# Kernel optimization log

Measured on AMD Instinct MI355X. Metric: run time of the kernel, lower is better.

## Reference

```python
import jax, jax.numpy as jnp
import numpy as np

D_MODEL = 1024
NUM_HEADS = 16
THETA = 10000.0


def _trunc_normal(key, shape):
    # matches torch.nn.init.trunc_normal_(std=std, a=-3*std, b=3*std)
    std = (2.0 / (shape[0] + shape[1])) ** 0.5
    return jax.random.truncated_normal(key, -3.0, 3.0, shape, dtype=jnp.float32) * std


def setup_inputs() -> dict:
    key = jax.random.key(0)
    kx, kq, kk, kv, ko = jax.random.split(key, 5)
    B, S, D = 2, 2048, D_MODEL
    return {
        "x": jax.random.normal(kx, (B, S, D), dtype=jnp.float32),
        "Wq": _trunc_normal(kq, (D, D)),  # torch Linear weight: [out, in]
        "Wk": _trunc_normal(kk, (D, D)),
        "Wv": _trunc_normal(kv, (D, D)),
        "Wo": _trunc_normal(ko, (D, D)),
        "token_positions": jnp.arange(S, dtype=jnp.int32),
    }


def _rope(x, token_positions):
    # x: [B, H, S, d_k]; RoPE on interleaved pairs (k r) with r=2
    d_k = x.shape[-1]
    inv_freq = THETA ** (-2.0 * jnp.arange(d_k // 2, dtype=jnp.float32) / d_k)
    ang = token_positions.astype(jnp.float32)[:, None] * inv_freq[None, :]  # [S, d_k/2]
    sin, cos = jnp.sin(ang).astype(x.dtype), jnp.cos(ang).astype(x.dtype)
    x0, x1 = x[..., 0::2], x[..., 1::2]
    y0 = x0 * cos - x1 * sin
    y1 = x0 * sin + x1 * cos
    return jnp.stack([y0, y1], axis=-1).reshape(x.shape)


def reference(x, Wq, Wk, Wv, Wo, token_positions):
    B, S, D = x.shape
    H = NUM_HEADS
    d_k = D // H

    def proj(W):  # y = x @ W^T, split heads -> [B, H, S, d_k]
        y = jnp.einsum('bsd,ed->bse', x, W)
        return y.reshape(B, S, H, d_k).transpose(0, 2, 1, 3)

    q = _rope(proj(Wq), token_positions)
    k = _rope(proj(Wk), token_positions)
    v = proj(Wv)

    # causal mask: attend where pos_k <= pos_q
    mask = token_positions[None, :] <= token_positions[:, None]  # [S_q, S_k]
    logits = jnp.einsum('bhqd,bhkd->bhqk', q, k) / (d_k ** 0.5)
    logits = jnp.where(mask, logits, -jnp.inf)
    scores = jax.nn.softmax(logits, axis=-1)
    attn = jnp.einsum('bhqk,bhkd->bhqd', scores, v)  # [B, H, S, d_k]
    attn = attn.transpose(0, 2, 1, 3).reshape(B, S, D)
    return jnp.einsum('bsd,ed->bse', attn, Wo)
```

## Files before the change

### kernel.cpp

```cpp
#include <hip/hip_runtime.h>
#include <hip/hip_bf16.h>

typedef __attribute__((ext_vector_type(8))) short s16x8;
typedef __attribute__((ext_vector_type(4))) float f32x4;

__device__ __forceinline__ unsigned short f2b(float x) {
  unsigned int u = __float_as_uint(x);
  u = (u + 0x7fffu + ((u >> 16) & 1u)) >> 16;
  return (unsigned short)u;
}

__device__ __forceinline__ float b2f(unsigned short u) {
  return __uint_as_float((unsigned int)u << 16);
}

__device__ __forceinline__ unsigned int cvtpk(float a, float b) {
  unsigned int r;
  asm("v_cvt_pk_bf16_f32 %0, %1, %2" : "=v"(r) : "v"(a), "v"(b));
  return r;
}

#if __has_builtin(__builtin_amdgcn_exp2f)
__device__ __forceinline__ float fexp2(float x) { return __builtin_amdgcn_exp2f(x); }
#else
__device__ __forceinline__ float fexp2(float x) { return exp2f(x); }
#endif

__device__ __forceinline__ void gl2lds16(const unsigned short* g, unsigned short* lds) {
  __builtin_amdgcn_global_load_lds(
      (const __attribute__((address_space(1))) unsigned int*)g,
      (__attribute__((address_space(3))) unsigned int*)lds, 16, 0, 0);
}

#define QSCALE 0.18033688011f

__global__ __launch_bounds__(256) void cast_all(
    const float* __restrict__ x,  const float* __restrict__ Wq,
    const float* __restrict__ Wk, const float* __restrict__ Wv,
    const float* __restrict__ Wo, unsigned short* __restrict__ dst) {
  int i = blockIdx.x * 256 + threadIdx.x;
  const float* src;
  int off;
  if (i < 1048576) { src = x; off = i; }
  else {
    int j = i - 1048576;
    int seg = j >> 18;
    off = j & 262143;
    src = (seg == 0) ? Wq : (seg == 1) ? Wk : (seg == 2) ? Wv : Wo;
  }
  const float4 v = ((const float4*)src)[off];
  uint2 o;
  o.x = cvtpk(v.x, v.y);
  o.y = cvtpk(v.z, v.w);
  ((uint2*)dst)[i] = o;
}

#define KDIM 1024

__global__ __launch_bounds__(256, 4) void gemm_qkv(
    const unsigned short* __restrict__ A,
    const unsigned short* __restrict__ Bt,
    const int* __restrict__ tok,
    unsigned short* __restrict__ Qo,
    unsigned short* __restrict__ Ko,
    unsigned short* __restrict__ Vt) {
  __shared__ unsigned short As[2][128 * 32];
  __shared__ unsigned short Bs[2][128 * 32];
  const int tid = threadIdx.x;
  const int bid = blockIdx.x;
  const int xcd = bid & 7;
  const int loc = bid >> 3;
  const int m0 = (loc / 3) * 128;
  const int n0 = (xcd * 3 + loc % 3) * 128;
  const int w = tid >> 6, lane = tid & 63;
  const int ln = lane & 15, quad = lane >> 4;
  const int wm = (w >> 1) * 64, wn = (w & 1) * 64;

  const int rr = lane >> 2;
  const int gsw = ((lane & 3) ^ ((rr ^ (rr >> 2)) & 3)) * 8;
  const int sr = (ln ^ (ln >> 2)) & 3;

  const f32x4 zero = {0.f, 0.f, 0.f, 0.f};
  f32x4 acc[4][4];
#pragma unroll
  for (int i = 0; i < 4; ++i)
#pragma unroll
    for (int j = 0; j < 4; ++j) acc[i][j] = zero;

#define QKV_STAGE(kb, p)                                                              \
  do {                                                                                \
    int col = (kb) * 32 + gsw;                                                        \
    gl2lds16(A  + (size_t)(m0 + w * 32 + rr) * KDIM + col,      &As[p][(w * 32) * 32]);      \
    gl2lds16(A  + (size_t)(m0 + w * 32 + 16 + rr) * KDIM + col, &As[p][(w * 32 + 16) * 32]); \
    gl2lds16(Bt + (size_t)(n0 + w * 32 + rr) * KDIM + col,      &Bs[p][(w * 32) * 32]);      \
    gl2lds16(Bt + (size_t)(n0 + w * 32 + 16 + rr) * KDIM + col, &Bs[p][(w * 32 + 16) * 32]); \
  } while (0)

  QKV_STAGE(0, 0);
  for (int kb = 0; kb < 32; ++kb) {
    const int p = kb & 1;
    __syncthreads();
    if (kb < 31) QKV_STAGE(kb + 1, p ^ 1);
    s16x8 af[4], bfr[4];
#pragma unroll
    for (int i = 0; i < 4; ++i)
      af[i] = *(const s16x8*)(&As[p][(wm + i * 16 + ln) * 32 + ((quad ^ sr) * 8)]);
#pragma unroll
    for (int j = 0; j < 4; ++j)
      bfr[j] = *(const s16x8*)(&Bs[p][(wn + j * 16 + ln) * 32 + ((quad ^ sr) * 8)]);
#pragma unroll
    for (int i = 0; i < 4; ++i)
#pragma unroll
      for (int j = 0; j < 4; ++j)
        acc[i][j] = __builtin_amdgcn_mfma_f32_16x16x32_bf16(af[i], bfr[j], acc[i][j], 0, 0, 0);
  }
#undef QKV_STAGE

  __syncthreads();
  const bool isV = (n0 >= 2048);
  if (!isV) {
    const float qs = (n0 + wn < 1024) ? QSCALE : 1.0f;
    const int gnb = n0 + wn;
    const int h = (gnb & 1023) >> 6;
    unsigned short* dst = (gnb < 1024) ? Qo : Ko;
    unsigned short* T = &As[0][0] + w * 1088;
    float invj[4];
#pragma unroll
    for (int j = 0; j < 4; ++j)
      invj[j] = __expf(-0.2878231366f * (float)((j * 16 + ln) >> 1));
#pragma unroll
    for (int i = 0; i < 4; ++i) {
      const int mb = m0 + wm + i * 16;
      const int b = mb >> 11;
      const int sb = mb & 2047;
#pragma unroll
      for (int j = 0; j < 4; ++j) {
        const int dd = j * 16 + ln;
#pragma unroll
        for (int r = 0; r < 4; ++r) {
          float val = acc[i][j][r];
          float part = __shfl_xor(val, 1, 64);
          int s = sb + quad * 4 + r;
          float ang = (float)s * invj[j];
          float sn, cs;
          __sincosf(ang, &sn, &cs);
          float x0 = (dd & 1) ? part : val;
          float x1 = (dd & 1) ? val : part;
          float y = (dd & 1) ? (x0 * sn + x1 * cs) : (x0 * cs - x1 * sn);
          T[(quad * 4 + r) * 68 + dd] = f2b(y * qs);
        }
      }
      __builtin_amdgcn_wave_barrier();
      const size_t obase = ((size_t)(b * 16 + h) * 2048 + sb) * 64;
#pragma unroll
      for (int ss = 0; ss < 16; ++ss)
        dst[obase + (size_t)ss * 64 + lane] = T[ss * 68 + lane];
      __builtin_amdgcn_wave_barrier();
    }
  } else {
    unsigned short* T = &As[0][0] + w * 1120;
    const int b = m0 >> 11;
    const int hrow = ((n0 - 2048) + wn) >> 6;
    const int s0 = (m0 & 2047) + wm;
    const size_t vbase = (size_t)(b * 16 + hrow) * 64;
#pragma unroll
    for (int j = 0; j < 4; ++j) {
#pragma unroll
      for (int i = 0; i < 4; ++i)
#pragma unroll
        for (int r = 0; r < 4; ++r)
          T[ln * 70 + i * 16 + quad * 4 + r] = f2b(acc[i][j][r]);
      __builtin_amdgcn_wave_barrier();
#pragma unroll
      for (int dd = 0; dd < 16; ++dd)
        Vt[(vbase + j * 16 + dd) * 2048 + s0 + lane] = T[dd * 70 + lane];
      __builtin_amdgcn_wave_barrier();
    }
  }
}

__global__ __launch_bounds__(256, 3) void attn_partial(
    const unsigned short* __restrict__ Q,
    const unsigned short* __restrict__ K,
    const unsigned short* __restrict__ Vt,
    unsigned short* __restrict__ Opart,
    float2* __restrict__ ML) {
  __shared__ unsigned short Ks[2][64 * 64];
  __shared__ unsigned short Vs[2][64 * 64];
  __shared__ unsigned short Pt[4][16 * 64];

  const int bid = blockIdx.x;
  const int xcd = bid & 7;
  const int loc = bid >> 3;
  const int bh = xcd * 4 + (loc & 3);
  const int widx = loc >> 2;
  int c, qh;
  if (widx < 28) {
    if (widx < 13)      { c = 0; qh = 3 + widx; }
    else if (widx < 22) { c = 1; qh = 7 + (widx - 13); }
    else if (widx < 27) { c = 2; qh = 11 + (widx - 22); }
    else                { c = 3; qh = 15; }
  } else {
    int s = widx - 28;
    int wt = s >> 2;
    c = s & 3;
    qh = 4 * c + 2 - wt;
  }
  const int kbeg = c * 512;
  const int khi = min(kbeg + 512, qh * 128 + 128);
  const int nit = (khi - kbeg) >> 6;

  const int tid = threadIdx.x;
  const int w = tid >> 6, lane = tid & 63;
  const int ln = lane & 15, quad = lane >> 4;
  const int qb = qh * 128 + w * 32;

  const unsigned short* Qb = Q + (size_t)bh * 2048 * 64;
  const unsigned short* Kb = K + (size_t)bh * 2048 * 64;
  const unsigned short* Vb = Vt + (size_t)bh * 64 * 2048;

  const int srow = w * 16 + (lane >> 3);
  const int sg = (lane & 7) ^ (srow & 7);

#define ATTN_STAGE(k0, p)                                                            \
  do {                                                                               \
    gl2lds16(Kb + (size_t)((k0) + srow) * 64 + sg * 8,       &Ks[p][(w * 16) * 64]);      \
    gl2lds16(Kb + (size_t)((k0) + srow + 8) * 64 + sg * 8,   &Ks[p][(w * 16 + 8) * 64]);  \
    gl2lds16(Vb + (size_t)srow * 2048 + (k0) + sg * 8,       &Vs[p][(w * 16) * 64]);      \
    gl2lds16(Vb + (size_t)(srow + 8) * 2048 + (k0) + sg * 8, &Vs[p][(w * 16 + 8) * 64]);  \
  } while (0)

  s16x8 bq[2][2];
#pragma unroll
  for (int u = 0; u < 2; ++u)
#pragma unroll
    for (int hh = 0; hh < 2; ++hh)
      bq[u][hh] = *(const s16x8*)(&Qb[(size_t)(qb + u * 16 + ln) * 64 + hh * 32 + quad * 8]);

  const f32x4 zero = {0.f, 0.f, 0.f, 0.f};
  f32x4 o[2][4];
#pragma unroll
  for (int u = 0; u < 2; ++u)
#pragma unroll
    for (int j = 0; j < 4; ++j) o[u][j] = zero;
  float m_i[2] = {-3e38f, -3e38f};
  float l_i[2] = {0.f, 0.f};

  const int rdsw = ((ln & 7) * 8);
  unsigned char* ptb = (unsigned char*)&Pt[w][0];
  const int pswz = (ln & 7) << 4;

  ATTN_STAGE(kbeg, 0);
  for (int it = 0; it < nit; ++it) {
    const int p = it & 1;
    const int k0 = kbeg + it * 64;
    __syncthreads();
    if (it + 1 < nit) ATTN_STAGE(k0 + 64, p ^ 1);

    if (k0 <= qb + 31) {
      s16x8 ka[4][2];
#pragma unroll
      for (int t = 0; t < 4; ++t)
#pragma unroll
        for (int hh = 0; hh < 2; ++hh)
          ka[t][hh] = *(const s16x8*)(&Ks[p][(t * 16 + ln) * 64 + (((hh * 4 + quad) * 8) ^ rdsw)]);

#pragma unroll
      for (int u = 0; u < 2; ++u) {
        const int qlo = qb + u * 16;
        if (k0 > qlo + 15) continue;
        f32x4 st[4];
#pragma unroll
        for (int t = 0; t < 4; ++t) {
          f32x4 s = __builtin_amdgcn_mfma_f32_16x16x32_bf16(ka[t][0], bq[u][0], zero, 0, 0, 0);
          st[t] = __builtin_amdgcn_mfma_f32_16x16x32_bf16(ka[t][1], bq[u][1], s, 0, 0, 0);
        }
        float lm = -3e38f;
        if (k0 + 63 > qlo) {
          const int q = qlo + ln;
#pragma unroll
          for (int t = 0; t < 4; ++t)
#pragma unroll
            for (int r = 0; r < 4; ++r) {
              int kk = k0 + t * 16 + quad * 4 + r;
              float v = st[t][r];
              v = (kk > q) ? -3e38f : v;
              st[t][r] = v;
              lm = fmaxf(lm, v);
            }
        } else {
#pragma unroll
          for (int t = 0; t < 4; ++t)
#pragma unroll
            for (int r = 0; r < 4; ++r) lm = fmaxf(lm, st[t][r]);
        }
        lm = fmaxf(lm, __shfl_xor(lm, 16, 64));
        lm = fmaxf(lm, __shfl_xor(lm, 32, 64));

        float rs = 0.f;
        if (__all(lm <= m_i[u])) {
          const float mn = m_i[u];
#pragma unroll
          for (int t = 0; t < 4; ++t)
#pragma unroll
            for (int r = 0; r < 4; ++r) {
              float pv = fexp2(st[t][r] - mn);
              st[t][r] = pv;
              rs += pv;
            }
          rs += __shfl_xor(rs, 16, 64);
          rs += __shfl_xor(rs, 32, 64);
          l_i[u] += rs;
        } else {
          const float mn = fmaxf(m_i[u], lm);
          const float al = fexp2(m_i[u] - mn);
#pragma unroll
          for (int t = 0; t < 4; ++t)
#pragma unroll
            for (int r = 0; r < 4; ++r) {
              float pv = fexp2(st[t][r] - mn);
              st[t][r] = pv;
              rs += pv;
            }
          rs += __shfl_xor(rs, 16, 64);
          rs += __shfl_xor(rs, 32, 64);
          m_i[u] = mn;
          l_i[u] = l_i[u] * al + rs;
#pragma unroll
          for (int j = 0; j < 4; ++j) o[u][j] *= al;
        }

#pragma unroll
        for (int t = 0; t < 4; ++t) {
          uint2 pv;
          pv.x = cvtpk(st[t][0], st[t][1]);
          pv.y = cvtpk(st[t][2], st[t][3]);
          *(uint2*)(ptb + ln * 128 + ((t * 32 + quad * 8) ^ pswz)) = pv;
        }
        __builtin_amdgcn_wave_barrier();
#pragma unroll
        for (int hh = 0; hh < 2; ++hh) {
          s16x8 pb = *(const s16x8*)(ptb + ln * 128 + ((hh * 64 + quad * 16) ^ pswz));
#pragma unroll
          for (int j = 0; j < 4; ++j) {
            s16x8 va = *(const s16x8*)(&Vs[p][(j * 16 + ln) * 64 + (((hh * 4 + quad) * 8) ^ rdsw)]);
            o[u][j] = __builtin_amdgcn_mfma_f32_16x16x32_bf16(va, pb, o[u][j], 0, 0, 0);
          }
        }
        __builtin_amdgcn_wave_barrier();
      }
    }
  }
#undef ATTN_STAGE

#pragma unroll
  for (int u = 0; u < 2; ++u) {
    int s = qb + u * 16 + ln;
    size_t row = ((size_t)bh * 4 + c) * 2048 + s;
    if (quad == 0) ML[row] = make_float2(m_i[u], l_i[u]);
    size_t base = row * 64;
#pragma unroll
    for (int j = 0; j < 4; ++j) {
      uint2 o4;
      o4.x = cvtpk(o[u][j][0], o[u][j][1]);
      o4.y = cvtpk(o[u][j][2], o[u][j][3]);
      *(uint2*)(&Opart[base + j * 16 + quad * 4]) = o4;
    }
  }
}

__global__ __launch_bounds__(256) void attn_merge(
    const unsigned short* __restrict__ Opart,
    const float2* __restrict__ ML,
    unsigned short* __restrict__ Ao) {
  int idx = blockIdx.x * 256 + threadIdx.x;
  int d0 = (idx & 7) * 8;
  int q  = (idx >> 3) & 2047;
  int bh = idx >> 14;
  int nc = (q >> 9) + 1;

  float m_c[4], l_c[4];
  float M = -3e38f;
  for (int c = 0; c < nc; ++c) {
    float2 ml = ML[((size_t)bh * 4 + c) * 2048 + q];
    m_c[c] = ml.x; l_c[c] = ml.y;
    M = fmaxf(M, ml.x);
  }
  float acc[8] = {0, 0, 0, 0, 0, 0, 0, 0};
  float L = 0.f;
  for (int c = 0; c < nc; ++c) {
    float wc = fexp2(m_c[c] - M);
    L += wc * l_c[c];
    const ushort4* p = (const ushort4*)(Opart + (((size_t)bh * 4 + c) * 2048 + q) * 64 + d0);
    ushort4 a = p[0], bvec = p[1];
    acc[0] += wc * b2f(a.x); acc[1] += wc * b2f(a.y);
    acc[2] += wc * b2f(a.z); acc[3] += wc * b2f(a.w);
    acc[4] += wc * b2f(bvec.x); acc[5] += wc * b2f(bvec.y);
    acc[6] += wc * b2f(bvec.z); acc[7] += wc * b2f(bvec.w);
  }
  float invL = 1.0f / L;
  int b = bh >> 4, h = bh & 15;
  unsigned short* dst = Ao + ((size_t)b * 2048 + q) * 1024 + h * 64 + d0;
  uint2 o0, o1;
  o0.x = cvtpk(acc[0] * invL, acc[1] * invL);
  o0.y = cvtpk(acc[2] * invL, acc[3] * invL);
  o1.x = cvtpk(acc[4] * invL, acc[5] * invL);
  o1.y = cvtpk(acc[6] * invL, acc[7] * invL);
  ((uint2*)dst)[0] = o0;
  ((uint2*)dst)[1] = o1;
}

__global__ __launch_bounds__(256, 3) void gemm_out(
    const unsigned short* __restrict__ A,
    const unsigned short* __restrict__ Bt,
    float* __restrict__ out) {
  __shared__ unsigned short As[128 * 64];
  __shared__ unsigned short Bs[128 * 64];
  const int tid = threadIdx.x;
  const int bid = blockIdx.x;
  const int m0 = (bid >> 3) * 128;
  const int n0 = (bid & 7) * 128;
  const int w = tid >> 6, lane = tid & 63;
  const int ln = lane & 15, quad = lane >> 4;
  const int wm = (w >> 1) * 64, wn = (w & 1) * 64;

  const int srow = w * 32 + (lane >> 3);
  const int sg = (lane & 7) ^ (lane >> 3);
  const int rs = ln & 7;

  const f32x4 zero = {0.f, 0.f, 0.f, 0.f};
  f32x4 acc[4][4];
#pragma unroll
  for (int i = 0; i < 4; ++i)
#pragma unroll
    for (int j = 0; j < 4; ++j) acc[i][j] = zero;

  for (int kb = 0; kb < KDIM / 64; ++kb) {
    __syncthreads();
#pragma unroll
    for (int t = 0; t < 4; ++t) {
      gl2lds16(A  + (size_t)(m0 + srow + t * 8) * KDIM + kb * 64 + sg * 8, &As[(w * 32 + t * 8) * 64]);
      gl2lds16(Bt + (size_t)(n0 + srow + t * 8) * KDIM + kb * 64 + sg * 8, &Bs[(w * 32 + t * 8) * 64]);
    }
    __syncthreads();
#pragma unroll
    for (int ks = 0; ks < 2; ++ks) {
      s16x8 af[4], bfr[4];
#pragma unroll
      for (int i = 0; i < 4; ++i)
        af[i] = *(const s16x8*)(&As[(wm + i * 16 + ln) * 64 + (((ks * 4 + quad) ^ rs) * 8)]);
#pragma unroll
      for (int j = 0; j < 4; ++j)
        bfr[j] = *(const s16x8*)(&Bs[(wn + j * 16 + ln) * 64 + (((ks * 4 + quad) ^ rs) * 8)]);
#pragma unroll
      for (int i = 0; i < 4; ++i)
#pragma unroll
        for (int j = 0; j < 4; ++j)
          acc[i][j] = __builtin_amdgcn_mfma_f32_16x16x32_bf16(af[i], bfr[j], acc[i][j], 0, 0, 0);
    }
  }
#pragma unroll
  for (int i = 0; i < 4; ++i) {
    int gmb = m0 + wm + i * 16 + quad * 4;
#pragma unroll
    for (int j = 0; j < 4; ++j) {
      int gn = n0 + wn + j * 16 + ln;
#pragma unroll
      for (int r = 0; r < 4; ++r)
        out[(size_t)(gmb + r) * 1024 + gn] = acc[i][j][r];
    }
  }
}

extern "C" void kernel_launch(void* const* d_in, const int* in_sizes, int n_in,
                              void* d_out, int out_size, void* d_ws, size_t ws_size,
                              hipStream_t stream) {
  const float* x  = (const float*)d_in[0];
  const float* Wq = (const float*)d_in[1];
  const float* Wk = (const float*)d_in[2];
  const float* Wv = (const float*)d_in[3];
  const float* Wo = (const float*)d_in[4];
  const int* tok  = (const int*)d_in[5];
  float* out = (float*)d_out;

  char* ws = (char*)d_ws;
  unsigned short* xb    = (unsigned short*)(ws);
  unsigned short* Wcat  = (unsigned short*)(ws + (8ull  << 20));
  unsigned short* Wob   = (unsigned short*)(ws + (14ull << 20));
  unsigned short* Qb    = (unsigned short*)(ws + (16ull << 20));
  unsigned short* Kb    = (unsigned short*)(ws + (24ull << 20));
  unsigned short* Vtb   = (unsigned short*)(ws + (32ull << 20));
  unsigned short* Ab    = (unsigned short*)(ws + (40ull << 20));
  unsigned short* Opart = (unsigned short*)(ws + (48ull << 20));
  float2*         ML    = (float2*)        (ws + (80ull << 20));

  cast_all<<<dim3(8192), dim3(256), 0, stream>>>(x, Wq, Wk, Wv, Wo, xb);
  gemm_qkv<<<dim3(768), dim3(256), 0, stream>>>(xb, Wcat, tok, Qb, Kb, Vtb);
  attn_partial<<<dim3(1280), dim3(256), 0, stream>>>(Qb, Kb, Vtb, Opart, ML);
  attn_merge<<<dim3(2048), dim3(256), 0, stream>>>(Opart, ML, Ab);
  gemm_out<<<dim3(256), dim3(256), 0, stream>>>(Ab, Wob, out);
}
```

Baseline: 184.3 us.

## Double-buffer LDS in output projection GEMM with BK=32 stages

Restructures the output-projection GEMM to use two LDS buffers of K-depth 32 instead of a single buffer of depth 64. The next stage is prefetched with global-to-LDS loads while the current one is consumed, which removes one barrier per iteration and overlaps memory with MFMA work. The LDS swizzle is redesigned for the 32-wide rows. The cost is twice as many iterations, each with fewer MFMAs per barrier. Correctness depends on the async LDS load completing before the barrier at the top of the next iteration.

```diff
diff --git a/kernel.cpp b/kernel.cpp
--- a/kernel.cpp
+++ b/kernel.cpp
@@ -414,8 +414,8 @@
     const unsigned short* __restrict__ A,
     const unsigned short* __restrict__ Bt,
     float* __restrict__ out) {
-  __shared__ unsigned short As[128 * 64];
-  __shared__ unsigned short Bs[128 * 64];
+  __shared__ unsigned short As[2][128 * 32];
+  __shared__ unsigned short Bs[2][128 * 32];
   const int tid = threadIdx.x;
   const int bid = blockIdx.x;
   const int m0 = (bid >> 3) * 128;
@@ -424,9 +424,9 @@
   const int ln = lane & 15, quad = lane >> 4;
   const int wm = (w >> 1) * 64, wn = (w & 1) * 64;
 
-  const int srow = w * 32 + (lane >> 3);
-  const int sg = (lane & 7) ^ (lane >> 3);
-  const int rs = ln & 7;
+  const int rr = lane >> 2;
+  const int gsw = ((lane & 3) ^ ((rr ^ (rr >> 2)) & 3)) * 8;
+  const int sr = (ln ^ (ln >> 2)) & 3;
 
   const f32x4 zero = {0.f, 0.f, 0.f, 0.f};
   f32x4 acc[4][4];
@@ -435,30 +435,35 @@
 #pragma unroll
     for (int j = 0; j < 4; ++j) acc[i][j] = zero;
 
-  for (int kb = 0; kb < KDIM / 64; ++kb) {
+#define OUT_STAGE(kb, p)                                                              \
+  do {                                                                                \
+    int col = (kb) * 32 + gsw;                                                        \
+    gl2lds16(A  + (size_t)(m0 + w * 32 + rr) * KDIM + col,      &As[p][(w * 32) * 32]);      \
+    gl2lds16(A  + (size_t)(m0 + w * 32 + 16 + rr) * KDIM + col, &As[p][(w * 32 + 16) * 32]); \
+    gl2lds16(Bt + (size_t)(n0 + w * 32 + rr) * KDIM + col,      &Bs[p][(w * 32) * 32]);      \
+    gl2lds16(Bt + (size_t)(n0 + w * 32 + 16 + rr) * KDIM + col, &Bs[p][(w * 32 + 16) * 32]); \
+  } while (0)
+
+  OUT_STAGE(0, 0);
+  for (int kb = 0; kb < 32; ++kb) {
+    const int p = kb & 1;
     __syncthreads();
-#pragma unroll
-    for (int t = 0; t < 4; ++t) {
-      gl2lds16(A  + (size_t)(m0 + srow + t * 8) * KDIM + kb * 64 + sg * 8, &As[(w * 32 + t * 8) * 64]);
-      gl2lds16(Bt + (size_t)(n0 + srow + t * 8) * KDIM + kb * 64 + sg * 8, &Bs[(w * 32 + t * 8) * 64]);
-    }
-    __syncthreads();
-#pragma unroll
-    for (int ks = 0; ks < 2; ++ks) {
-      s16x8 af[4], bfr[4];
-#pragma unroll
-      for (int i = 0; i < 4; ++i)
-        af[i] = *(const s16x8*)(&As[(wm + i * 16 + ln) * 64 + (((ks * 4 + quad) ^ rs) * 8)]);
+    if (kb < 31) OUT_STAGE(kb + 1, p ^ 1);
+    s16x8 af[4], bfr[4];
+#pragma unroll
+    for (int i = 0; i < 4; ++i)
+      af[i] = *(const s16x8*)(&As[p][(wm + i * 16 + ln) * 32 + ((quad ^ sr) * 8)]);
+#pragma unroll
+    for (int j = 0; j < 4; ++j)
+      bfr[j] = *(const s16x8*)(&Bs[p][(wn + j * 16 + ln) * 32 + ((quad ^ sr) * 8)]);
+#pragma unroll
+    for (int i = 0; i < 4; ++i)
 #pragma unroll
       for (int j = 0; j < 4; ++j)
-        bfr[j] = *(const s16x8*)(&Bs[(wn + j * 16 + ln) * 64 + (((ks * 4 + quad) ^ rs) * 8)]);
-#pragma unroll
-      for (int i = 0; i < 4; ++i)
-#pragma unroll
-        for (int j = 0; j < 4; ++j)
-          acc[i][j] = __builtin_amdgcn_mfma_f32_16x16x32_bf16(af[i], bfr[j], acc[i][j], 0, 0, 0);
-    }
-  }
+        acc[i][j] = __builtin_amdgcn_mfma_f32_16x16x32_bf16(af[i], bfr[j], acc[i][j], 0, 0, 0);
+  }
+#undef OUT_STAGE
+
 #pragma unroll
   for (int i = 0; i < 4; ++i) {
     int gmb = m0 + wm + i * 16 + quad * 4;
```

Result: no change. 186.8 us (+1.3%).
